# Kernel optimization log

Measured on AMD Instinct MI355X. Metric: run time of the kernel, lower is better.

## Reference

```python
import jax, jax.numpy as jnp
import numpy as np

# mamba-130m config (n_layers reduced to 4 for the reference baseline)
V, Dm, NL, Di, Ns, K, R = 50280, 768, 4, 1536, 16, 4, 48

def rmsnorm(x, w, eps=1e-5):
    return x * jax.lax.rsqrt(jnp.mean(x * x, axis=-1, keepdims=True) + eps) * w

def mixer(r, in_w, conv_w, conv_b, x_w, dt_w, dt_b, A_log, Dp, out_w):
    Bsz, L, _ = r.shape
    xz = jnp.einsum('bld,ed->ble', r, in_w)            # [B,L,2*Di]
    x, z = jnp.split(xz, 2, axis=-1)
    # depthwise causal conv1d, kernel K
    xp = jnp.pad(x, ((0, 0), (K - 1, 0), (0, 0)))
    x = sum(conv_w[:, k] * xp[:, k:k + L] for k in range(K)) + conv_b
    x = jax.nn.silu(x)
    proj = jnp.einsum('bld,ed->ble', x, x_w)           # [B,L,R+2*Ns]
    dt_r, Bm, Cm = proj[..., :R], proj[..., R:R + Ns], proj[..., R + Ns:]
    dt = jax.nn.softplus(jnp.einsum('blr,dr->bld', dt_r, dt_w) + dt_b)  # [B,L,Di]
    A = -jnp.exp(A_log)                                # [Di,Ns]
    dA = jnp.exp(dt[..., None] * A)                    # [B,L,Di,Ns]
    dBx = dt[..., None] * Bm[:, :, None, :] * x[..., None]
    def step(h, xs):
        dA_t, dBx_t, C_t = xs
        h = dA_t * h + dBx_t                           # [B,Di,Ns]
        return h, jnp.einsum('bdn,bn->bd', h, C_t)
    h0 = jnp.zeros((Bsz, Di, Ns), r.dtype)
    _, ys = jax.lax.scan(step, h0, (dA.transpose(1, 0, 2, 3), dBx.transpose(1, 0, 2, 3), Cm.transpose(1, 0, 2)))
    y = ys.transpose(1, 0, 2) + Dp * x
    y = y * jax.nn.silu(z)
    return jnp.einsum('ble,de->bld', y, out_w)

def mamba_logits(ids, mask, embed, in_proj_w, conv_w, conv_b, x_proj_w, dt_proj_w, dt_proj_b, A_log, Dp, out_proj_w, norm_w, final_norm_w):
    h = embed[ids] * mask[..., None].astype(embed.dtype)
    for l in range(NL):
        h = h + mixer(rmsnorm(h, norm_w[l]), in_proj_w[l], conv_w[l], conv_b[l],
                      x_proj_w[l], dt_proj_w[l], dt_proj_b[l], A_log[l], Dp[l], out_proj_w[l])
    h = rmsnorm(h, final_norm_w)
    return jnp.einsum('bld,vd->blv', h, embed)  # tied lm_head

def setup_inputs() -> dict:
    key = jax.random.key(0)
    ks = jax.random.split(key, 12)
    s = 0.02
    B, Lq, La = 2, 512, 128
    dt_b0 = float(np.log(np.expm1(0.01)))  # softplus^{-1}(0.01)
    return {
        'question_ids': jax.random.randint(ks[0], (B, Lq), 0, V, dtype=jnp.int64),
        'question_mask': jnp.ones((B, Lq), dtype=jnp.int32),
        'answer_ids': jax.random.randint(ks[1], (B, La), 0, V, dtype=jnp.int64),
        'answer_mask': jnp.ones((B, La), dtype=jnp.int32),
        'embed': jax.random.normal(ks[2], (V, Dm), jnp.float32) * s,
        'in_proj_w': jax.random.normal(ks[3], (NL, 2 * Di, Dm), jnp.float32) * s,
        'conv_w': jax.random.normal(ks[4], (NL, Di, K), jnp.float32) * s,
        'conv_b': jnp.zeros((NL, Di), jnp.float32),
        'x_proj_w': jax.random.normal(ks[5], (NL, R + 2 * Ns, Di), jnp.float32) * s,
        'dt_proj_w': jax.random.normal(ks[6], (NL, Di, R), jnp.float32) * s,
        'dt_proj_b': jnp.full((NL, Di), dt_b0, jnp.float32),
        'A_log': jnp.broadcast_to(jnp.log(jnp.arange(1, Ns + 1, dtype=jnp.float32)), (NL, Di, Ns)).copy(),
        'Dp': jnp.ones((NL, Di), jnp.float32),
        'out_proj_w': jax.random.normal(ks[7], (NL, Dm, Di), jnp.float32) * s,
        'norm_w': jnp.ones((NL, Dm), jnp.float32),
        'final_norm_w': jnp.ones((Dm,), jnp.float32),
    }

def reference(question_ids, question_mask, answer_ids, answer_mask, embed, in_proj_w, conv_w, conv_b, x_proj_w, dt_proj_w, dt_proj_b, A_log, Dp, out_proj_w, norm_w, final_norm_w):
    # answer_ids/answer_mask are unused by the original forward as well.
    return mamba_logits(question_ids, question_mask, embed, in_proj_w, conv_w, conv_b,
                        x_proj_w, dt_proj_w, dt_proj_b, A_log, Dp, out_proj_w, norm_w, final_norm_w)
```

## Files before the change

### kernel.cpp

```cpp
#include <hip/hip_runtime.h>

#define DI 1536
#define DM 768
#define NS 16
#define RK 48
#define LQ 512
#define BB 2
#define MROWS (BB*LQ)

typedef short bf16x8 __attribute__((ext_vector_type(8)));
typedef float f32x4 __attribute__((ext_vector_type(4)));

static __device__ __forceinline__ short f2bf(float f) {
  unsigned u = __float_as_uint(f);
  u += 0x7FFF + ((u >> 16) & 1);
  return (short)(u >> 16);
}

__global__ __launch_bounds__(256) void k_gather(const int* __restrict__ ids,
                                                const int* __restrict__ mask,
                                                const float* __restrict__ embed,
                                                float* __restrict__ h) {
  int row = blockIdx.x;
  int id = ids[row];
  float mk = (float)mask[row];
  const float* src = embed + (size_t)id * DM;
  float* dst = h + (size_t)row * DM;
  for (int i = threadIdx.x; i < DM; i += 256) dst[i] = src[i] * mk;
}

__global__ __launch_bounds__(256) void k_rmsnorm(const float* __restrict__ h,
                                                 const float* __restrict__ w,
                                                 float* __restrict__ out) {
  int row = blockIdx.x;
  const float* x = h + (size_t)row * DM;
  int tid = threadIdx.x;
  float v0 = x[tid], v1 = x[tid + 256], v2 = x[tid + 512];
  float ss = v0*v0 + v1*v1 + v2*v2;
  #pragma unroll
  for (int o = 32; o > 0; o >>= 1) ss += __shfl_xor(ss, o);
  __shared__ float ps[4];
  if ((tid & 63) == 0) ps[tid >> 6] = ss;
  __syncthreads();
  float tot = ps[0] + ps[1] + ps[2] + ps[3];
  float scale = rsqrtf(tot * (1.0f/768.0f) + 1e-5f);
  float* o0 = out + (size_t)row * DM;
  o0[tid]       = v0 * scale * w[tid];
  o0[tid + 256] = v1 * scale * w[tid + 256];
  o0[tid + 512] = v2 * scale * w[tid + 512];
}

template<int TM, int TN, bool RES>
__global__ __launch_bounds__(256) void k_gemm_nt(const float* __restrict__ A,
                                                 const float* __restrict__ B,
                                                 float* __restrict__ C,
                                                 int M, int N, int K) {
  constexpr int BM = TM*32, BN = TN*32, BK = 32, SK = 40;
  __shared__ short As[BM*SK];
  __shared__ short Bs[BN*SK];

  int bx, by;
  {
    const int GC = 96;
    int CT = gridDim.x, RT = gridDim.y;
    int lin = blockIdx.y * CT + blockIdx.x;
    int panel = GC * RT;
    int grp = lin / panel;
    int rem = lin - grp * panel;
    int c0 = grp * GC;
    int gc = CT - c0; if (gc > GC) gc = GC;
    by = rem % RT;
    bx = c0 + rem / RT;
  }

  const int m0 = by * BM, n0 = bx * BN;
  const int tid = threadIdx.x;
  const int wave = tid >> 6, lane = tid & 63;
  const int wm = (wave >> 1) * (TM*16), wn = (wave & 1) * (TN*16);
  const int lm = lane & 15, q = lane >> 4;
  const int trow = tid >> 3;
  const int tcol = (tid & 7) * 4;
  f32x4 acc[TM][TN] = {};
  for (int kt = 0; kt < K; kt += BK) {
    float4 av[TM], bv[TN];
    #pragma unroll
    for (int p = 0; p < TM; p++)
      av[p] = *(const float4*)(A + (size_t)(m0 + p*32 + trow)*K + kt + tcol);
    #pragma unroll
    for (int p = 0; p < TN; p++) {
      int bn = n0 + p*32 + trow;
      bv[p] = (bn < N) ? *(const float4*)(B + (size_t)bn*K + kt + tcol)
                       : make_float4(0.f, 0.f, 0.f, 0.f);
    }
    __syncthreads();
    #pragma unroll
    for (int p = 0; p < TM; p++) {
      short4 s; s.x = f2bf(av[p].x); s.y = f2bf(av[p].y); s.z = f2bf(av[p].z); s.w = f2bf(av[p].w);
      *(short4*)(&As[(p*32 + trow)*SK + tcol]) = s;
    }
    #pragma unroll
    for (int p = 0; p < TN; p++) {
      short4 s; s.x = f2bf(bv[p].x); s.y = f2bf(bv[p].y); s.z = f2bf(bv[p].z); s.w = f2bf(bv[p].w);
      *(short4*)(&Bs[(p*32 + trow)*SK + tcol]) = s;
    }
    __syncthreads();
    bf16x8 af[TM], bfr[TN];
    #pragma unroll
    for (int i = 0; i < TM; i++)
      af[i] = *(const bf16x8*)(&As[(wm + i*16 + lm)*SK + q*8]);
    #pragma unroll
    for (int j = 0; j < TN; j++)
      bfr[j] = *(const bf16x8*)(&Bs[(wn + j*16 + lm)*SK + q*8]);
    #pragma unroll
    for (int i = 0; i < TM; i++)
      #pragma unroll
      for (int j = 0; j < TN; j++)
        acc[i][j] = __builtin_amdgcn_mfma_f32_16x16x32_bf16(af[i], bfr[j], acc[i][j], 0, 0, 0);
  }
  #pragma unroll
  for (int i = 0; i < TM; i++) {
    #pragma unroll
    for (int j = 0; j < TN; j++) {
      int rm = m0 + wm + i*16 + q*4;
      int cn = n0 + wn + j*16 + lm;
      if (cn < N) {
        float* cp = C + (size_t)rm*N + cn;
        #pragma unroll
        for (int r2 = 0; r2 < 4; r2++) {
          float v = acc[i][j][r2];
          if (RES) v += cp[(size_t)r2*N];
          cp[(size_t)r2*N] = v;
        }
      }
    }
  }
}

__global__ __launch_bounds__(256) void k_conv(const float* __restrict__ xz,
                                              const float* __restrict__ cw,
                                              const float* __restrict__ cb,
                                              float* __restrict__ xs) {
  int idx = blockIdx.x * 256 + threadIdx.x;
  int d = idx % DI;
  int t = (idx / DI) % LQ;
  int b = idx / (DI * LQ);
  const float* xcol = xz + (size_t)b * LQ * (2*DI) + d;
  float acc = cb[d];
  #pragma unroll
  for (int k = 0; k < 4; k++) {
    int tt = t + k - 3;
    if (tt >= 0) acc += cw[d*4 + k] * xcol[(size_t)tt * (2*DI)];
  }
  float s = acc / (1.0f + expf(-acc));
  xs[idx] = s;
}

__global__ __launch_bounds__(256) void k_proj(const float* __restrict__ xs,
                                              const float* __restrict__ w,
                                              float* __restrict__ proj) {
  int wave = threadIdx.x >> 6, lane = threadIdx.x & 63;
  int m = blockIdx.x * 4 + wave;
  const float* xr = xs + (size_t)m * DI;
  float xv[24];
  #pragma unroll
  for (int j = 0; j < 24; j++) xv[j] = xr[lane + j*64];
  for (int n = 0; n < 80; n++) {
    const float* wr = w + (size_t)n * DI;
    float acc = 0.f;
    #pragma unroll
    for (int j = 0; j < 24; j++) acc += xv[j] * wr[lane + j*64];
    #pragma unroll
    for (int o = 32; o > 0; o >>= 1) acc += __shfl_xor(acc, o);
    if (lane == 0) proj[(size_t)m * 80 + n] = acc;
  }
}

__global__ __launch_bounds__(256) void k_dt(const float* __restrict__ proj,
                                            const float* __restrict__ dtw,
                                            const float* __restrict__ dtb,
                                            float* __restrict__ dt) {
  int m = blockIdx.y;
  int d = blockIdx.x * 256 + threadIdx.x;
  __shared__ float p[RK];
  if (threadIdx.x < RK) p[threadIdx.x] = proj[(size_t)m * 80 + threadIdx.x];
  __syncthreads();
  const float* wr = dtw + (size_t)d * RK;
  float acc = dtb[d];
  #pragma unroll
  for (int r = 0; r < RK; r++) acc += p[r] * wr[r];
  float sp = (acc > 20.f) ? acc : log1pf(expf(acc));
  dt[(size_t)m * DI + d] = sp;
}

#define SCT 32
__global__ __launch_bounds__(256) void k_scan(const float* __restrict__ dt,
                                              const float* __restrict__ proj,
                                              const float* __restrict__ xs,
                                              const float* __restrict__ A_log,
                                              float* __restrict__ y) {
  const int d = blockIdx.x;
  const int b = blockIdx.y;
  const int tid = threadIdx.x;
  const int n = tid & 15;
  const int c = tid >> 4;
  const int t0 = c * SCT;
  const float negA = -expf(A_log[d * NS + n]);
  const float* dtp = dt   + (size_t)b * LQ * DI + d;
  const float* xp  = xs   + (size_t)b * LQ * DI + d;
  const float* Bp  = proj + (size_t)b * LQ * 80 + RK + n;
  const float* Cp  = proj + (size_t)b * LQ * 80 + RK + NS + n;

  float a[SCT], u[SCT], Cv[SCT];
  #pragma unroll
  for (int j = 0; j < SCT; j++) {
    int t = t0 + j;
    float dtv = dtp[(size_t)t * DI];
    float xv  = xp[(size_t)t * DI];
    float Bv  = Bp[(size_t)t * 80];
    Cv[j]     = Cp[(size_t)t * 80];
    a[j] = expf(dtv * negA);
    u[j] = dtv * Bv * xv;
  }
  float P = 1.f, H = 0.f;
  #pragma unroll
  for (int j = 0; j < SCT; j++) { H = a[j]*H + u[j]; P *= a[j]; }

  __shared__ float Ps[16][16], Hs[16][16], Ss[16][16];
  Ps[c][n] = P; Hs[c][n] = H;
  __syncthreads();
  if (tid < 16) {
    float S = 0.f;
    #pragma unroll
    for (int cc = 0; cc < 16; cc++) {
      Ss[cc][tid] = S;
      S = Ps[cc][tid] * S + Hs[cc][tid];
    }
  }
  __syncthreads();

  float h = Ss[c][n];
  float* yp = y + (size_t)b * LQ * DI + d;
  #pragma unroll
  for (int j = 0; j < SCT; j++) {
    h = a[j]*h + u[j];
    float yy = h * Cv[j];
    yy += __shfl_xor(yy, 1);
    yy += __shfl_xor(yy, 2);
    yy += __shfl_xor(yy, 4);
    yy += __shfl_xor(yy, 8);
    if (n == 0) yp[(size_t)(t0 + j) * DI] = yy;
  }
}

__global__ __launch_bounds__(256) void k_gate(float* __restrict__ y,
                                              const float* __restrict__ xs,
                                              const float* __restrict__ xz,
                                              const float* __restrict__ Dp) {
  int idx = blockIdx.x * 256 + threadIdx.x;
  int d = idx % DI;
  int bt = idx / DI;
  float zv = xz[(size_t)bt * (2*DI) + DI + d];
  float sz = zv / (1.0f + expf(-zv));
  y[idx] = (y[idx] + Dp[d] * xs[idx]) * sz;
}

extern "C" void kernel_launch(void* const* d_in, const int* in_sizes, int n_in,
                              void* d_out, int out_size, void* d_ws, size_t ws_size,
                              hipStream_t stream) {
  const int*   q_ids        = (const int*)d_in[0];
  const int*   q_mask       = (const int*)d_in[1];
  const float* embed        = (const float*)d_in[4];
  const float* in_proj_w    = (const float*)d_in[5];
  const float* conv_w       = (const float*)d_in[6];
  const float* conv_b       = (const float*)d_in[7];
  const float* x_proj_w     = (const float*)d_in[8];
  const float* dt_proj_w    = (const float*)d_in[9];
  const float* dt_proj_b    = (const float*)d_in[10];
  const float* A_log        = (const float*)d_in[11];
  const float* Dp           = (const float*)d_in[12];
  const float* out_proj_w   = (const float*)d_in[13];
  const float* norm_w       = (const float*)d_in[14];
  const float* final_norm_w = (const float*)d_in[15];
  float* out = (float*)d_out;

  float* ws = (float*)d_ws;
  float* h   = ws;
  float* r   = h  + 786432;
  float* xz  = r  + 786432;
  float* xs  = xz + 3145728;
  float* pj  = xs + 1572864;
  float* dtb = pj + 81920;
  float* y   = dtb + 1572864;

  k_gather<<<MROWS, 256, 0, stream>>>(q_ids, q_mask, embed, h);

  for (int l = 0; l < 4; l++) {
    k_rmsnorm<<<MROWS, 256, 0, stream>>>(h, norm_w + (size_t)l*DM, r);
    k_gemm_nt<2,4,false><<<dim3(3072/128, MROWS/64), 256, 0, stream>>>(
        r, in_proj_w + (size_t)l*2*DI*DM, xz, MROWS, 2*DI, DM);
    k_conv<<<(MROWS*DI)/256, 256, 0, stream>>>(xz, conv_w + (size_t)l*DI*4,
                                               conv_b + (size_t)l*DI, xs);
    k_proj<<<MROWS/4, 256, 0, stream>>>(xs, x_proj_w + (size_t)l*80*DI, pj);
    k_dt<<<dim3(DI/256, MROWS), 256, 0, stream>>>(pj, dt_proj_w + (size_t)l*DI*RK,
                                                  dt_proj_b + (size_t)l*DI, dtb);
    k_scan<<<dim3(DI, BB), 256, 0, stream>>>(dtb, pj, xs,
                                             A_log + (size_t)l*DI*NS, y);
    k_gate<<<(MROWS*DI)/256, 256, 0, stream>>>(y, xs, xz, Dp + (size_t)l*DI);
    k_gemm_nt<2,2,true><<<dim3(DM/64, MROWS/64), 256, 0, stream>>>(
        y, out_proj_w + (size_t)l*DM*DI, h, MROWS, DM, DI);
  }

  k_rmsnorm<<<MROWS, 256, 0, stream>>>(h, final_norm_w, r);
  k_gemm_nt<4,4,false><<<dim3((50280 + 127)/128, MROWS/128), 256, 0, stream>>>(
      r, embed, out, MROWS, 50280, 768);
}
```

Before: 1.675 ms.

## Pre-cast GEMM operands to bf16 and stage tiles via direct global-to-LDS loads

Adds a cast kernel that converts the in_proj, out_proj and embedding weights to bf16 on every call. RMSNorm and the gate kernel now write bf16 activations, and the GEMM loads bf16 tiles straight into LDS with global_load_lds. This halves operand bytes and removes the per-tile fp32-to-bf16 conversion and the register staging inside the GEMM. The trade-offs are about 53M extra floats read and written per call by the cast kernels, an LDS layout without padding that may cause bank conflicts, and a new tile swizzle.

```diff
diff --git a/kernel.cpp b/kernel.cpp
--- a/kernel.cpp
+++ b/kernel.cpp
@@ -8,13 +8,33 @@
 #define BB 2
 #define MROWS (BB*LQ)
 
+typedef unsigned short u16;
 typedef short bf16x8 __attribute__((ext_vector_type(8)));
 typedef float f32x4 __attribute__((ext_vector_type(4)));
+typedef u16 u16x8 __attribute__((ext_vector_type(8)));
 
 static __device__ __forceinline__ short f2bf(float f) {
   unsigned u = __float_as_uint(f);
   u += 0x7FFF + ((u >> 16) & 1);
   return (short)(u >> 16);
+}
+
+static __device__ __forceinline__ void gld16(const void* g, void* l) {
+  __builtin_amdgcn_global_load_lds((const __attribute__((address_space(1))) unsigned int*)g,
+                                   (__attribute__((address_space(3))) unsigned int*)l,
+                                   16, 0, 0);
+}
+
+__global__ __launch_bounds__(256) void k_cast8(const float* __restrict__ s,
+                                               u16* __restrict__ d, long n) {
+  long i = ((long)blockIdx.x * 256 + threadIdx.x) * 8;
+  if (i >= n) return;
+  float4 a = *(const float4*)(s + i);
+  float4 b = *(const float4*)(s + i + 4);
+  u16x8 o;
+  o[0] = (u16)f2bf(a.x); o[1] = (u16)f2bf(a.y); o[2] = (u16)f2bf(a.z); o[3] = (u16)f2bf(a.w);
+  o[4] = (u16)f2bf(b.x); o[5] = (u16)f2bf(b.y); o[6] = (u16)f2bf(b.z); o[7] = (u16)f2bf(b.w);
+  *(u16x8*)(d + i) = o;
 }
 
 __global__ __launch_bounds__(256) void k_gather(const int* __restrict__ ids,
@@ -31,7 +51,7 @@
 
 __global__ __launch_bounds__(256) void k_rmsnorm(const float* __restrict__ h,
                                                  const float* __restrict__ w,
-                                                 float* __restrict__ out) {
+                                                 u16* __restrict__ out) {
   int row = blockIdx.x;
   const float* x = h + (size_t)row * DM;
   int tid = threadIdx.x;
@@ -44,73 +64,69 @@
   __syncthreads();
   float tot = ps[0] + ps[1] + ps[2] + ps[3];
   float scale = rsqrtf(tot * (1.0f/768.0f) + 1e-5f);
-  float* o0 = out + (size_t)row * DM;
-  o0[tid]       = v0 * scale * w[tid];
-  o0[tid + 256] = v1 * scale * w[tid + 256];
-  o0[tid + 512] = v2 * scale * w[tid + 512];
-}
-
-template<int TM, int TN, bool RES>
-__global__ __launch_bounds__(256) void k_gemm_nt(const float* __restrict__ A,
-                                                 const float* __restrict__ B,
+  u16* o0 = out + (size_t)row * DM;
+  o0[tid]       = (u16)f2bf(v0 * scale * w[tid]);
+  o0[tid + 256] = (u16)f2bf(v1 * scale * w[tid + 256]);
+  o0[tid + 512] = (u16)f2bf(v2 * scale * w[tid + 512]);
+}
+
+template<int WM, int WN, int TM, int TN, bool RES>
+__global__ __launch_bounds__(256) void k_gemm_bf(const u16* __restrict__ A,
+                                                 const u16* __restrict__ B,
                                                  float* __restrict__ C,
                                                  int M, int N, int K) {
-  constexpr int BM = TM*32, BN = TN*32, BK = 32, SK = 40;
-  __shared__ short As[BM*SK];
-  __shared__ short Bs[BN*SK];
+  constexpr int BM = WM*TM*16, BN = WN*TN*16, BK = 32;
+  __shared__ __attribute__((aligned(16))) u16 As[BM*BK];
+  __shared__ __attribute__((aligned(16))) u16 Bs[BN*BK];
 
   int bx, by;
   {
-    const int GC = 96;
     int CT = gridDim.x, RT = gridDim.y;
     int lin = blockIdx.y * CT + blockIdx.x;
-    int panel = GC * RT;
-    int grp = lin / panel;
-    int rem = lin - grp * panel;
-    int c0 = grp * GC;
-    int gc = CT - c0; if (gc > GC) gc = GC;
-    by = rem % RT;
-    bx = c0 + rem / RT;
+    int CT8 = CT & ~7;
+    int main_n = CT8 * RT;
+    if (lin < main_n) {
+      int x = lin & 7, g = lin >> 3;
+      by = g % RT;
+      bx = x + 8 * (g / RT);
+    } else {
+      int rem = lin - main_n;
+      by = rem % RT;
+      bx = CT8 + rem / RT;
+    }
   }
 
   const int m0 = by * BM, n0 = bx * BN;
   const int tid = threadIdx.x;
   const int wave = tid >> 6, lane = tid & 63;
-  const int wm = (wave >> 1) * (TM*16), wn = (wave & 1) * (TN*16);
+  const int wm = (wave / WN) * (TM*16), wn = (wave % WN) * (TN*16);
   const int lm = lane & 15, q = lane >> 4;
-  const int trow = tid >> 3;
-  const int tcol = (tid & 7) * 4;
+  const int srow = tid >> 2;
+  const int ssub = (tid & 3) * 8;
+
   f32x4 acc[TM][TN] = {};
   for (int kt = 0; kt < K; kt += BK) {
-    float4 av[TM], bv[TN];
-    #pragma unroll
-    for (int p = 0; p < TM; p++)
-      av[p] = *(const float4*)(A + (size_t)(m0 + p*32 + trow)*K + kt + tcol);
-    #pragma unroll
-    for (int p = 0; p < TN; p++) {
-      int bn = n0 + p*32 + trow;
-      bv[p] = (bn < N) ? *(const float4*)(B + (size_t)bn*K + kt + tcol)
-                       : make_float4(0.f, 0.f, 0.f, 0.f);
-    }
     __syncthreads();
     #pragma unroll
-    for (int p = 0; p < TM; p++) {
-      short4 s; s.x = f2bf(av[p].x); s.y = f2bf(av[p].y); s.z = f2bf(av[p].z); s.w = f2bf(av[p].w);
-      *(short4*)(&As[(p*32 + trow)*SK + tcol]) = s;
-    }
-    #pragma unroll
-    for (int p = 0; p < TN; p++) {
-      short4 s; s.x = f2bf(bv[p].x); s.y = f2bf(bv[p].y); s.z = f2bf(bv[p].z); s.w = f2bf(bv[p].w);
-      *(short4*)(&Bs[(p*32 + trow)*SK + tcol]) = s;
+    for (int i = 0; i < BM/64; i++) {
+      const u16* g = A + (size_t)(m0 + i*64 + srow)*K + kt + ssub;
+      gld16(g, (void*)(As + (i*256 + wave*64)*8));
+    }
+    #pragma unroll
+    for (int i = 0; i < BN/64; i++) {
+      int bn = n0 + i*64 + srow;
+      if (bn > N-1) bn = N-1;
+      const u16* g = B + (size_t)bn*K + kt + ssub;
+      gld16(g, (void*)(Bs + (i*256 + wave*64)*8));
     }
     __syncthreads();
     bf16x8 af[TM], bfr[TN];
     #pragma unroll
     for (int i = 0; i < TM; i++)
-      af[i] = *(const bf16x8*)(&As[(wm + i*16 + lm)*SK + q*8]);
+      af[i] = *(const bf16x8*)(&As[(wm + i*16 + lm)*BK + q*8]);
     #pragma unroll
     for (int j = 0; j < TN; j++)
-      bfr[j] = *(const bf16x8*)(&Bs[(wn + j*16 + lm)*SK + q*8]);
+      bfr[j] = *(const bf16x8*)(&Bs[(wn + j*16 + lm)*BK + q*8]);
     #pragma unroll
     for (int i = 0; i < TM; i++)
       #pragma unroll
@@ -252,16 +268,18 @@
   }
 }
 
-__global__ __launch_bounds__(256) void k_gate(float* __restrict__ y,
+__global__ __launch_bounds__(256) void k_gate(const float* __restrict__ y,
                                               const float* __restrict__ xs,
                                               const float* __restrict__ xz,
-                                              const float* __restrict__ Dp) {
+                                              const float* __restrict__ Dp,
+                                              u16* __restrict__ yb) {
   int idx = blockIdx.x * 256 + threadIdx.x;
   int d = idx % DI;
   int bt = idx / DI;
   float zv = xz[(size_t)bt * (2*DI) + DI + d];
   float sz = zv / (1.0f + expf(-zv));
-  y[idx] = (y[idx] + Dp[d] * xs[idx]) * sz;
+  float v = (y[idx] + Dp[d] * xs[idx]) * sz;
+  yb[idx] = (u16)f2bf(v);
 }
 
 extern "C" void kernel_launch(void* const* d_in, const int* in_sizes, int n_in,
@@ -285,19 +303,27 @@
 
   float* ws = (float*)d_ws;
   float* h   = ws;
-  float* r   = h  + 786432;
-  float* xz  = r  + 786432;
+  float* xz  = h  + 786432;
   float* xs  = xz + 3145728;
   float* pj  = xs + 1572864;
   float* dtb = pj + 81920;
   float* y   = dtb + 1572864;
+  u16*   rb  = (u16*)(y + 1572864);
+  u16*   yb  = rb  + 786432;
+  u16*   ipw = yb  + 1572864;
+  u16*   opw = ipw + 9437184;
+  u16*   emb = opw + 4718592;
+
+  k_cast8<<<4608, 256, 0, stream>>>(in_proj_w, ipw, 9437184L);
+  k_cast8<<<2304, 256, 0, stream>>>(out_proj_w, opw, 4718592L);
+  k_cast8<<<18855, 256, 0, stream>>>(embed, emb, 38615040L);
 
   k_gather<<<MROWS, 256, 0, stream>>>(q_ids, q_mask, embed, h);
 
   for (int l = 0; l < 4; l++) {
-    k_rmsnorm<<<MROWS, 256, 0, stream>>>(h, norm_w + (size_t)l*DM, r);
-    k_gemm_nt<2,4,false><<<dim3(3072/128, MROWS/64), 256, 0, stream>>>(
-        r, in_proj_w + (size_t)l*2*DI*DM, xz, MROWS, 2*DI, DM);
+    k_rmsnorm<<<MROWS, 256, 0, stream>>>(h, norm_w + (size_t)l*DM, rb);
+    k_gemm_bf<1,4,4,2,false><<<dim3(3072/128, MROWS/64), 256, 0, stream>>>(
+        rb, ipw + (size_t)l*2359296, xz, MROWS, 2*DI, DM);
     k_conv<<<(MROWS*DI)/256, 256, 0, stream>>>(xz, conv_w + (size_t)l*DI*4,
                                                conv_b + (size_t)l*DI, xs);
     k_proj<<<MROWS/4, 256, 0, stream>>>(xs, x_proj_w + (size_t)l*80*DI, pj);
@@ -305,12 +331,12 @@
                                                   dt_proj_b + (size_t)l*DI, dtb);
     k_scan<<<dim3(DI, BB), 256, 0, stream>>>(dtb, pj, xs,
                                              A_log + (size_t)l*DI*NS, y);
-    k_gate<<<(MROWS*DI)/256, 256, 0, stream>>>(y, xs, xz, Dp + (size_t)l*DI);
-    k_gemm_nt<2,2,true><<<dim3(DM/64, MROWS/64), 256, 0, stream>>>(
-        y, out_proj_w + (size_t)l*DM*DI, h, MROWS, DM, DI);
-  }
-
-  k_rmsnorm<<<MROWS, 256, 0, stream>>>(h, final_norm_w, r);
-  k_gemm_nt<4,4,false><<<dim3((50280 + 127)/128, MROWS/128), 256, 0, stream>>>(
-      r, embed, out, MROWS, 50280, 768);
-}
+    k_gate<<<(MROWS*DI)/256, 256, 0, stream>>>(y, xs, xz, Dp + (size_t)l*DI, yb);
+    k_gemm_bf<2,2,2,2,true><<<dim3(DM/64, MROWS/64), 256, 0, stream>>>(
+        yb, opw + (size_t)l*1179648, h, MROWS, DM, DI);
+  }
+
+  k_rmsnorm<<<MROWS, 256, 0, stream>>>(h, final_norm_w, rb);
+  k_gemm_bf<2,2,4,4,false><<<dim3((50280 + 127)/128, MROWS/128), 256, 0, stream>>>(
+      rb, emb, out, MROWS, 50280, 768);
+}
```

Result: faster. 1.537 ms (-8.2%).
